# Kernel tuning notes

Hardware: AMD Instinct MI355X
Metric: run time of the kernel (lower is better)

Reference implementation:

```python
import jax, jax.numpy as jnp
import numpy as np

# Block sizes: 3-hop sampled bipartite graphs (src -> dst per layer)
N_SRC0, N_DST0, E0 = 500_000, 100_000, 1_000_000
N_DST1, E1 = 10_000, 100_000
N_DST2, E2 = 1_024, 10_240
D_IN, D_HID, N_CLS = 128, 128, 47


def setup_inputs() -> dict:
    key = jax.random.key(0)
    ks = jax.random.split(key, 16)
    feats = jax.random.normal(ks[0], (N_SRC0, D_IN), dtype=jnp.float32)
    src0 = jax.random.randint(ks[1], (E0,), 0, N_SRC0)
    dst0 = jax.random.randint(ks[2], (E0,), 0, N_DST0)
    src1 = jax.random.randint(ks[3], (E1,), 0, N_DST0)
    dst1 = jax.random.randint(ks[4], (E1,), 0, N_DST1)
    src2 = jax.random.randint(ks[5], (E2,), 0, N_DST1)
    dst2 = jax.random.randint(ks[6], (E2,), 0, N_DST2)
    # fsi.inverse_idx reindex + NPFeatureShuffle all-to-all -> two permutations
    inverse_idx = jax.random.permutation(ks[7], N_DST0)
    shuffle_idx = jax.random.permutation(ks[8], N_DST0)
    def glorot(k, fan_in, fan_out):
        lim = np.sqrt(6.0 / (fan_in + fan_out)).astype(np.float32)
        return jax.random.uniform(k, (fan_in, fan_out), jnp.float32, -lim, lim)
    W0 = glorot(ks[9], D_IN, D_HID)
    b0 = jnp.zeros((D_HID,), jnp.float32)
    W1 = glorot(ks[10], D_HID, D_HID)
    b1 = jnp.zeros((D_HID,), jnp.float32)
    W2 = glorot(ks[11], D_HID, N_CLS)
    b2 = jnp.zeros((N_CLS,), jnp.float32)
    return dict(feats=feats, src0=src0, dst0=dst0, src1=src1, dst1=dst1,
                src2=src2, dst2=dst2, inverse_idx=inverse_idx,
                shuffle_idx=shuffle_idx, W0=W0, b0=b0, W1=W1, b1=b1, W2=W2, b2=b2)


def _graph_conv(h_src, src, dst, n_src, n_dst, W, b, norm_both):
    # DGL GraphConv: optional D^{-1/2} on src, W, sum-aggregate over edges,
    # optional D^{-1/2} on dst, + bias. Degrees clamped to min 1.
    ones = jnp.ones(src.shape[0], dtype=h_src.dtype)
    if norm_both:
        out_deg = jax.ops.segment_sum(ones, src, num_segments=n_src)
        h_src = h_src * jax.lax.rsqrt(jnp.clip(out_deg, 1.0, None))[:, None]
    msgs = (h_src @ W)[src]                      # [E, d_out] gather
    agg = jax.ops.segment_sum(msgs, dst, num_segments=n_dst)  # scatter-add
    if norm_both:
        in_deg = jax.ops.segment_sum(ones, dst, num_segments=n_dst)
        agg = agg * jax.lax.rsqrt(jnp.clip(in_deg, 1.0, None))[:, None]
    return agg + b


def reference(feats, src0, dst0, src1, dst1, src2, dst2,
              inverse_idx, shuffle_idx, W0, b0, W1, b1, W2, b2):
    # layer 0: norm='none'
    h = _graph_conv(feats, src0, dst0, N_SRC0, N_DST0, W0, b0, norm_both=False)
    # fsi.inverse_idx reindex + NPFeatureShuffle (modeled as permutations)
    h = h[inverse_idx]
    h = h[shuffle_idx]
    h = jax.nn.relu(h)  # dropout is identity in eval
    # layer 1: norm='both'
    h = _graph_conv(h, src1, dst1, N_DST0, N_DST1, W1, b1, norm_both=True)
    h = jax.nn.relu(h)
    # layer 2: norm='both'
    h = _graph_conv(h, src2, dst2, N_DST1, N_DST2, W2, b2, norm_both=True)
    return h
```

## Files before the change

kernel.cpp:

```cpp
#include <hip/hip_runtime.h>
#include <stdint.h>

typedef unsigned int u32;
typedef unsigned short u16;
typedef __attribute__((ext_vector_type(8))) short short8;
typedef __attribute__((ext_vector_type(4))) float f32x4;

#define N_SRC0 500000
#define N_DST0 100000
#define N_DST1 10000
#define N_DST2 1024
#define NCLS 47
#define CAP 64

static __device__ __forceinline__ float bf16_lo(u32 v) { return __uint_as_float(v << 16); }
static __device__ __forceinline__ float bf16_hi(u32 v) { return __uint_as_float(v & 0xffff0000u); }
static __device__ __forceinline__ float bf16_to_f(u16 s) { return __uint_as_float(((u32)s) << 16); }
static __device__ __forceinline__ u16 f_to_bf16(float f) {
    u32 u = __float_as_uint(f);
    u32 r = u + 0x7fffu + ((u >> 16) & 1u);
    return (u16)(r >> 16);
}

#define OFF_X1     0u
#define OFF_X2     51200000u
#define OFF_CSR0   56320000u
#define OFF_CSR1   81920000u
#define OFF_CSR2   84480000u
#define OFF_CNT0   84742144u
#define OFF_DS1    85142144u
#define OFF_CNT1   85542144u
#define OFF_DS2    85582144u
#define OFF_CNT2   85622144u
#define ZERO_OFF   OFF_CNT0
#define ZERO_N4    55256u
#define OFF_WF0    85626240u
#define OFF_WF1    85691776u
#define OFF_WC2    85757312u
#define OFF_BC0    85781376u
#define OFF_BC1    85781888u
#define OFF_BC2    85782400u
#define OFF_FLAG   85782656u

__global__ __launch_bounds__(256) void k_prep(
    const u32* __restrict__ feats_w,
    const void* __restrict__ W0, const void* __restrict__ b0,
    const void* __restrict__ W1, const void* __restrict__ b1,
    const void* __restrict__ W2, const void* __restrict__ b2,
    float4* __restrict__ zbase,
    u16* __restrict__ wf0, u16* __restrict__ wf1,
    float* __restrict__ wc2, float* __restrict__ bc0,
    float* __restrict__ bc1, float* __restrict__ bc2,
    u32* __restrict__ flag)
{
    int b = blockIdx.x, t = threadIdx.x;
    if (b < 216) {
        u32 i = b * 256 + t;
        if (i < ZERO_N4) zbase[i] = make_float4(0.f, 0.f, 0.f, 0.f);
        return;
    }
    if (b == 216) {
        if (t < 64) {
            u32 u = feats_w[t];
            int e = (u >> 23) & 0xff;
            unsigned long long m = __ballot(e >= 0xC0);
            if (t == 0) *flag = (m != 0ull) ? 1u : 0u;
        }
        return;
    }
    __shared__ u32 lflag;
    if (b < 233) {
        const void* W = (b < 225) ? W0 : W1;
        u16* dst = (b < 225) ? wf0 : wf1;
        int base = ((b < 225) ? (b - 217) : (b - 225)) * 256;
        if (t == 0) lflag = 0u;
        __syncthreads();
        if (t < 64) { u32 u = ((const u32*)W)[t]; if (((u >> 23) & 0xff) >= 0xC0) atomicOr(&lflag, 1u); }
        __syncthreads();
        bool bf = (lflag != 0u);
        int idx = base + t;
        int fid = idx >> 6, lane = idx & 63;
        int nt = fid >> 2, ks = fid & 3;
        #pragma unroll
        for (int j = 0; j < 8; ++j) {
            int k = ks * 32 + (lane >> 4) * 8 + j;
            int n = nt * 16 + (lane & 15);
            u16 v = bf ? ((const u16*)W)[k * 128 + n]
                       : f_to_bf16(((const float*)W)[k * 128 + n]);
            dst[idx * 8 + j] = v;
        }
        return;
    }
    if (b < 257) {
        if (t == 0) lflag = 0u;
        __syncthreads();
        if (t < 64) { u32 u = ((const u32*)W2)[t]; if (((u >> 23) & 0xff) >= 0xC0) atomicOr(&lflag, 1u); }
        __syncthreads();
        bool bf = (lflag != 0u);
        int i = (b - 233) * 256 + t;
        if (i < 128 * NCLS)
            wc2[i] = bf ? bf16_to_f(((const u16*)W2)[i]) : ((const float*)W2)[i];
        return;
    }
    if (t < 128) { bc0[t] = ((const float*)b0)[t]; bc1[t] = ((const float*)b1)[t]; }
    if (t < NCLS) bc2[t] = ((const float*)b2)[t];
}

__global__ __launch_bounds__(256) void k_build(
    const int* __restrict__ src0, const int* __restrict__ dst0,
    const int* __restrict__ src1, const int* __restrict__ dst1,
    const int* __restrict__ src2, const int* __restrict__ dst2,
    u32* __restrict__ cnt0, int* __restrict__ csr0,
    u32* __restrict__ dS1,
    u32* __restrict__ cnt1, int* __restrict__ csr1,
    u32* __restrict__ dS2,
    u32* __restrict__ cnt2, int* __restrict__ csr2,
    int E0, int E1, int E2)
{
    int i = blockIdx.x * 256 + threadIdx.x;
    if (i < E0) {
        int d = dst0[i];
        u32 slot = atomicAdd(&cnt0[d], 1u);
        if (slot < CAP) csr0[d * CAP + slot] = src0[i];
    }
    if (i < E1) {
        atomicAdd(&dS1[src1[i]], 1u);
        int d = dst1[i];
        u32 slot = atomicAdd(&cnt1[d], 1u);
        if (slot < CAP) csr1[d * CAP + slot] = src1[i];
    }
    if (i < E2) {
        atomicAdd(&dS2[src2[i]], 1u);
        int d = dst2[i];
        u32 slot = atomicAdd(&cnt2[d], 1u);
        if (slot < CAP) csr2[d * CAP + slot] = src2[i];
    }
}

__global__ __launch_bounds__(256) void k_layer(
    const void* __restrict__ Ain, const u32* __restrict__ flag,
    const u32* __restrict__ cnt, const int* __restrict__ csr,
    const int* __restrict__ inv, const int* __restrict__ shuf,
    const u32* __restrict__ preDeg, const u32* __restrict__ postDeg,
    const u16* __restrict__ Wfrag, const float* __restrict__ bias,
    float* __restrict__ out, int rows)
{
    __shared__ u16  As[48][136];
    __shared__ u32  eS[48], degS[48];
    __shared__ float preS[48], postS[48], bS[128];

    int tid = threadIdx.x;
    int wv = tid >> 6, lane = tid & 63;
    int I0 = blockIdx.x * 48;

    if (tid < 48) {
        int I = I0 + tid;
        u32 e0 = 0u, dg = 0u; float pre = 1.f, post = 1.f;
        if (I < rows) {
            int ar = shuf ? inv[shuf[I]] : I;
            u32 c = cnt[ar];
            e0 = (u32)ar * CAP;
            dg = c < (u32)CAP ? c : (u32)CAP;
            if (preDeg)  { u32 d = preDeg[I];  pre  = rsqrtf((float)(d > 1u ? d : 1u)); }
            if (postDeg) { u32 d = postDeg[I]; post = rsqrtf((float)(d > 1u ? d : 1u)); }
        }
        eS[tid] = e0; degS[tid] = dg; preS[tid] = pre; postS[tid] = post;
    }
    if (tid < 128) bS[tid] = bias[tid];
    __syncthreads();

    bool bfp = flag && (*flag != 0u);

    for (int i = 0; i < 12; i += 3) {
        int rA = wv * 12 + i, rB = rA + 1, rC = rA + 2;
        int eA = (int)__builtin_amdgcn_readfirstlane(eS[rA]);
        int eB = (int)__builtin_amdgcn_readfirstlane(eS[rB]);
        int eC = (int)__builtin_amdgcn_readfirstlane(eS[rC]);
        int dA = (int)__builtin_amdgcn_readfirstlane(degS[rA]);
        int dB = (int)__builtin_amdgcn_readfirstlane(degS[rB]);
        int dC = (int)__builtin_amdgcn_readfirstlane(degS[rC]);
        int md = dA > dB ? dA : dB; md = md > dC ? md : dC;

        float xA = 0.f, yA = 0.f, xB = 0.f, yB = 0.f, xC = 0.f, yC = 0.f;

        if (bfp) {
            const u32* F = (const u32*)Ain;
            for (int k = 0; k < md; k += 8) {
                u32 vA[8], vB[8], vC[8];
                #pragma unroll
                for (int j = 0; j < 8; ++j) {
                    vA[j] = 0u;
                    if (k + j < dA) { int s = csr[eA + k + j]; vA[j] = F[(size_t)s * 64 + lane]; }
                }
                #pragma unroll
                for (int j = 0; j < 8; ++j) {
                    vB[j] = 0u;
                    if (k + j < dB) { int s = csr[eB + k + j]; vB[j] = F[(size_t)s * 64 + lane]; }
                }
                #pragma unroll
                for (int j = 0; j < 8; ++j) {
                    vC[j] = 0u;
                    if (k + j < dC) { int s = csr[eC + k + j]; vC[j] = F[(size_t)s * 64 + lane]; }
                }
                #pragma unroll
                for (int j = 0; j < 8; ++j) {
                    xA += bf16_lo(vA[j]); yA += bf16_hi(vA[j]);
                    xB += bf16_lo(vB[j]); yB += bf16_hi(vB[j]);
                    xC += bf16_lo(vC[j]); yC += bf16_hi(vC[j]);
                }
            }
        } else {
            const float2* F = (const float2*)Ain;
            for (int k = 0; k < md; k += 8) {
                float2 vA[8], vB[8], vC[8];
                #pragma unroll
                for (int j = 0; j < 8; ++j) {
                    vA[j] = make_float2(0.f, 0.f);
                    if (k + j < dA) { int s = csr[eA + k + j]; vA[j] = F[(size_t)s * 64 + lane]; }
                }
                #pragma unroll
                for (int j = 0; j < 8; ++j) {
                    vB[j] = make_float2(0.f, 0.f);
                    if (k + j < dB) { int s = csr[eB + k + j]; vB[j] = F[(size_t)s * 64 + lane]; }
                }
                #pragma unroll
                for (int j = 0; j < 8; ++j) {
                    vC[j] = make_float2(0.f, 0.f);
                    if (k + j < dC) { int s = csr[eC + k + j]; vC[j] = F[(size_t)s * 64 + lane]; }
                }
                #pragma unroll
                for (int j = 0; j < 8; ++j) {
                    xA += vA[j].x; yA += vA[j].y;
                    xB += vB[j].x; yB += vB[j].y;
                    xC += vC[j].x; yC += vC[j].y;
                }
            }
        }

        u32 pkA = ((u32)f_to_bf16(yA) << 16) | (u32)f_to_bf16(xA);
        u32 pkB = ((u32)f_to_bf16(yB) << 16) | (u32)f_to_bf16(xB);
        u32 pkC = ((u32)f_to_bf16(yC) << 16) | (u32)f_to_bf16(xC);
        *(u32*)&As[rA][2 * lane] = pkA;
        *(u32*)&As[rB][2 * lane] = pkB;
        *(u32*)&As[rC][2 * lane] = pkC;
    }

    short8 bfr[2][4];
    #pragma unroll
    for (int nt = 0; nt < 2; ++nt)
        #pragma unroll
        for (int ks = 0; ks < 4; ++ks) {
            int fid = (wv * 2 + nt) * 4 + ks;
            bfr[nt][ks] = *(const short8*)(Wfrag + (size_t)(fid * 64 + lane) * 8);
        }
    __syncthreads();

    f32x4 acc[2][3];
    #pragma unroll
    for (int nt = 0; nt < 2; ++nt)
        #pragma unroll
        for (int mt = 0; mt < 3; ++mt) acc[nt][mt] = (f32x4){0.f, 0.f, 0.f, 0.f};

    #pragma unroll
    for (int ks = 0; ks < 4; ++ks) {
        short8 af[3];
        #pragma unroll
        for (int mt = 0; mt < 3; ++mt) {
            int row = mt * 16 + (lane & 15);
            int k0 = ks * 32 + (lane >> 4) * 8;
            af[mt] = *(const short8*)&As[row][k0];
        }
        #pragma unroll
        for (int nt = 0; nt < 2; ++nt)
            #pragma unroll
            for (int mt = 0; mt < 3; ++mt)
                acc[nt][mt] = __builtin_amdgcn_mfma_f32_16x16x32_bf16(
                    af[mt], bfr[nt][ks], acc[nt][mt], 0, 0, 0);
    }

    int quad = lane >> 4, cl = lane & 15;
    #pragma unroll
    for (int nt = 0; nt < 2; ++nt) {
        int col = (wv * 2 + nt) * 16 + cl;
        float bb = bS[col];
        #pragma unroll
        for (int mt = 0; mt < 3; ++mt) {
            #pragma unroll
            for (int rg = 0; rg < 4; ++rg) {
                int lr = mt * 16 + quad * 4 + rg;
                int I = I0 + lr;
                if (I < rows) {
                    float v = acc[nt][mt][rg] * preS[lr] + bb;
                    v = v > 0.f ? v : 0.f;
                    out[(size_t)I * 128 + col] = v * postS[lr];
                }
            }
        }
    }
}

__global__ __launch_bounds__(256) void k_layer2(
    const float2* __restrict__ x2, const u32* __restrict__ cnt,
    const int* __restrict__ csr, const u32* __restrict__ preDeg,
    const float* __restrict__ Wc2, const float* __restrict__ bc2,
    void* __restrict__ out, const u32* __restrict__ flag)
{
    __shared__ float t2[16][128];
    int tid = threadIdx.x;
    int wv = tid >> 6, lane = tid & 63;
    int R0 = blockIdx.x * 16;

    for (int i = 0; i < 4; ++i) {
        int r = wv * 4 + i;
        int R = R0 + r;
        float x = 0.f, y = 0.f;
        u32 c = cnt[R];
        u32 e = (u32)R * CAP, end = e + (c < (u32)CAP ? c : (u32)CAP);
        for (; e + 4 <= end; e += 4) {
            int s0 = csr[e], s1 = csr[e+1], s2 = csr[e+2], s3 = csr[e+3];
            float2 v0 = x2[(size_t)s0 * 64 + lane];
            float2 v1 = x2[(size_t)s1 * 64 + lane];
            float2 v2 = x2[(size_t)s2 * 64 + lane];
            float2 v3 = x2[(size_t)s3 * 64 + lane];
            x += v0.x + v1.x + v2.x + v3.x;
            y += v0.y + v1.y + v2.y + v3.y;
        }
        for (; e < end; ++e) {
            float2 v = x2[(size_t)csr[e] * 64 + lane];
            x += v.x; y += v.y;
        }
        t2[r][2 * lane] = x;
        t2[r][2 * lane + 1] = y;
    }
    __syncthreads();

    bool bfp = flag && (*flag != 0u);
    for (int idx = tid; idx < 16 * NCLS; idx += 256) {
        int r = idx / NCLS, c = idx - NCLS * r;
        float a = 0.f;
        #pragma unroll 8
        for (int k = 0; k < 128; ++k) a = fmaf(t2[r][k], Wc2[k * NCLS + c], a);
        u32 d = preDeg[R0 + r];
        float v = a * rsqrtf((float)(d > 1u ? d : 1u)) + bc2[c];
        int g = (R0 + r) * NCLS + c;
        if (bfp) ((u16*)out)[g] = f_to_bf16(v);
        else     ((float*)out)[g] = v;
    }
}

extern "C" void kernel_launch(void* const* d_in, const int* in_sizes, int n_in,
                              void* d_out, int out_size, void* d_ws, size_t ws_size,
                              hipStream_t stream)
{
    (void)n_in; (void)out_size; (void)ws_size;
    const void* feats = d_in[0];
    const int* src0 = (const int*)d_in[1];
    const int* dst0 = (const int*)d_in[2];
    const int* src1 = (const int*)d_in[3];
    const int* dst1 = (const int*)d_in[4];
    const int* src2 = (const int*)d_in[5];
    const int* dst2 = (const int*)d_in[6];
    const int* inv  = (const int*)d_in[7];
    const int* shuf = (const int*)d_in[8];
    const void* W0 = d_in[9];  const void* b0 = d_in[10];
    const void* W1 = d_in[11]; const void* b1 = d_in[12];
    const void* W2 = d_in[13]; const void* b2 = d_in[14];
    int E0 = in_sizes[1], E1 = in_sizes[3], E2 = in_sizes[5];

    char* ws = (char*)d_ws;
    float* x1  = (float*)(ws + OFF_X1);
    float* x2  = (float*)(ws + OFF_X2);
    int* csr0 = (int*)(ws + OFF_CSR0);
    int* csr1 = (int*)(ws + OFF_CSR1);
    int* csr2 = (int*)(ws + OFF_CSR2);
    u32* cnt0 = (u32*)(ws + OFF_CNT0);
    u32* dS1  = (u32*)(ws + OFF_DS1);
    u32* cnt1 = (u32*)(ws + OFF_CNT1);
    u32* dS2  = (u32*)(ws + OFF_DS2);
    u32* cnt2 = (u32*)(ws + OFF_CNT2);
    u16* wf0  = (u16*)(ws + OFF_WF0);
    u16* wf1  = (u16*)(ws + OFF_WF1);
    float* wc2 = (float*)(ws + OFF_WC2);
    float* bc0 = (float*)(ws + OFF_BC0);
    float* bc1 = (float*)(ws + OFF_BC1);
    float* bc2 = (float*)(ws + OFF_BC2);
    u32* flag  = (u32*)(ws + OFF_FLAG);

    k_prep<<<258, 256, 0, stream>>>((const u32*)feats, W0, b0, W1, b1, W2, b2,
                                    (float4*)(ws + ZERO_OFF), wf0, wf1, wc2,
                                    bc0, bc1, bc2, flag);
    k_build<<<(E0 + 255) / 256, 256, 0, stream>>>(
        src0, dst0, src1, dst1, src2, dst2,
        cnt0, csr0, dS1, cnt1, csr1, dS2, cnt2, csr2, E0, E1, E2);
    k_layer<<<(N_DST0 + 47) / 48, 256, 0, stream>>>(
        feats, flag, cnt0, csr0, inv, shuf, nullptr, dS1, wf0, bc0, x1, N_DST0);
    k_layer<<<(N_DST1 + 47) / 48, 256, 0, stream>>>(
        x1, nullptr, cnt1, csr1, nullptr, nullptr, cnt1, dS2, wf1, bc1, x2, N_DST1);
    k_layer2<<<N_DST2 / 16, 256, 0, stream>>>(
        (const float2*)x2, cnt2, csr2, cnt2, wc2, bc2, d_out, flag);
}
```

Measured before the change: 554.3 us.

## Reorder layers to transform-then-aggregate with bf16 intermediate features

Splits each fused aggregate-then-GEMM layer into a dense GEMM kernel that projects every source row to bf16 first, followed by a gather/aggregate kernel that applies bias, ReLU and degree normalisation. The gathers for layers 0 and 1 now read bf16 projected rows instead of the raw inputs. The layer-1 activations are also stored as bf16 rather than fp32. In exchange the GEMM now runs over all 500k source rows instead of the 100k destinations, and the workspace grows by a large extra projected buffer, which adds streaming traffic.

```diff
diff --git a/kernel.cpp b/kernel.cpp
--- a/kernel.cpp
+++ b/kernel.cpp
@@ -22,25 +22,27 @@
     return (u16)(r >> 16);
 }
 
-#define OFF_X1     0u
-#define OFF_X2     51200000u
-#define OFF_CSR0   56320000u
-#define OFF_CSR1   81920000u
-#define OFF_CSR2   84480000u
-#define OFF_CNT0   84742144u
-#define OFF_DS1    85142144u
-#define OFF_CNT1   85542144u
-#define OFF_DS2    85582144u
-#define OFF_CNT2   85622144u
+#define OFF_Y0     0u
+#define OFF_X1     128004096u
+#define OFF_Y1     153604096u
+#define OFF_X2     179204096u
+#define OFF_CSR0   184324096u
+#define OFF_CSR1   209924096u
+#define OFF_CSR2   212484096u
+#define OFF_CNT0   212746240u
+#define OFF_DS1    213146240u
+#define OFF_CNT1   213546240u
+#define OFF_DS2    213586240u
+#define OFF_CNT2   213626240u
 #define ZERO_OFF   OFF_CNT0
 #define ZERO_N4    55256u
-#define OFF_WF0    85626240u
-#define OFF_WF1    85691776u
-#define OFF_WC2    85757312u
-#define OFF_BC0    85781376u
-#define OFF_BC1    85781888u
-#define OFF_BC2    85782400u
-#define OFF_FLAG   85782656u
+#define OFF_WF0    213630336u
+#define OFF_WF1    213695872u
+#define OFF_WC2    213761408u
+#define OFF_BC0    213785472u
+#define OFF_BC1    213785984u
+#define OFF_BC2    213786496u
+#define OFF_FLAG   213786752u
 
 __global__ __launch_bounds__(256) void k_prep(
     const u32* __restrict__ feats_w,
@@ -137,20 +139,104 @@
     }
 }
 
-__global__ __launch_bounds__(256) void k_layer(
-    const void* __restrict__ Ain, const u32* __restrict__ flag,
+__global__ __launch_bounds__(256) void k_gemm(
+    const void* __restrict__ Xin, const u32* __restrict__ flag, int isBf16In,
+    const u16* __restrict__ Wfrag, u16* __restrict__ Yout, int rows)
+{
+    __shared__ u16 As[48][136];
+    int tid = threadIdx.x, wv = tid >> 6, lane = tid & 63;
+    int I0 = blockIdx.x * 48;
+    bool bfp = flag ? (*flag != 0u) : (isBf16In != 0);
+
+    if (bfp) {
+        const uint4* F = (const uint4*)Xin;
+        for (int t = tid; t < 48 * 16; t += 256) {
+            int r = t >> 4, c = t & 15;
+            int I = I0 + r;
+            uint4 v = make_uint4(0u, 0u, 0u, 0u);
+            if (I < rows) v = F[(size_t)I * 16 + c];
+            *(uint4*)&As[r][c * 8] = v;
+        }
+    } else {
+        const float4* F = (const float4*)Xin;
+        for (int t = tid; t < 48 * 32; t += 256) {
+            int r = t >> 5, c = t & 31;
+            int I = I0 + r;
+            float4 v = make_float4(0.f, 0.f, 0.f, 0.f);
+            if (I < rows) v = F[(size_t)I * 32 + c];
+            u32 lo = ((u32)f_to_bf16(v.y) << 16) | (u32)f_to_bf16(v.x);
+            u32 hi = ((u32)f_to_bf16(v.w) << 16) | (u32)f_to_bf16(v.z);
+            *(u32*)&As[r][c * 4]     = lo;
+            *(u32*)&As[r][c * 4 + 2] = hi;
+        }
+    }
+
+    short8 bfr[2][4];
+    #pragma unroll
+    for (int nt = 0; nt < 2; ++nt)
+        #pragma unroll
+        for (int ks = 0; ks < 4; ++ks) {
+            int fid = (wv * 2 + nt) * 4 + ks;
+            bfr[nt][ks] = *(const short8*)(Wfrag + (size_t)(fid * 64 + lane) * 8);
+        }
+    __syncthreads();
+
+    f32x4 acc[2][3];
+    #pragma unroll
+    for (int nt = 0; nt < 2; ++nt)
+        #pragma unroll
+        for (int mt = 0; mt < 3; ++mt) acc[nt][mt] = (f32x4){0.f, 0.f, 0.f, 0.f};
+
+    #pragma unroll
+    for (int ks = 0; ks < 4; ++ks) {
+        short8 af[3];
+        #pragma unroll
+        for (int mt = 0; mt < 3; ++mt) {
+            int row = mt * 16 + (lane & 15);
+            int k0 = ks * 32 + (lane >> 4) * 8;
+            af[mt] = *(const short8*)&As[row][k0];
+        }
+        #pragma unroll
+        for (int nt = 0; nt < 2; ++nt)
+            #pragma unroll
+            for (int mt = 0; mt < 3; ++mt)
+                acc[nt][mt] = __builtin_amdgcn_mfma_f32_16x16x32_bf16(
+                    af[mt], bfr[nt][ks], acc[nt][mt], 0, 0, 0);
+    }
+    __syncthreads();
+
+    int quad = lane >> 4, cl = lane & 15;
+    #pragma unroll
+    for (int nt = 0; nt < 2; ++nt) {
+        int col = (wv * 2 + nt) * 16 + cl;
+        #pragma unroll
+        for (int mt = 0; mt < 3; ++mt)
+            #pragma unroll
+            for (int rg = 0; rg < 4; ++rg)
+                As[mt * 16 + quad * 4 + rg][col] = f_to_bf16(acc[nt][mt][rg]);
+    }
+    __syncthreads();
+
+    for (int t = tid; t < 48 * 16; t += 256) {
+        int r = t >> 4, c = t & 15;
+        int I = I0 + r;
+        if (I < rows)
+            *(uint4*)&Yout[(size_t)I * 128 + c * 8] = *(const uint4*)&As[r][c * 8];
+    }
+}
+
+__global__ __launch_bounds__(256) void k_agg(
+    const u32* __restrict__ Y,
     const u32* __restrict__ cnt, const int* __restrict__ csr,
     const int* __restrict__ inv, const int* __restrict__ shuf,
     const u32* __restrict__ preDeg, const u32* __restrict__ postDeg,
-    const u16* __restrict__ Wfrag, const float* __restrict__ bias,
-    float* __restrict__ out, int rows)
-{
-    __shared__ u16  As[48][136];
+    const float* __restrict__ bias, void* __restrict__ outp,
+    int outBf16, int rows)
+{
     __shared__ u32  eS[48], degS[48];
-    __shared__ float preS[48], postS[48], bS[128];
-
-    int tid = threadIdx.x;
-    int wv = tid >> 6, lane = tid & 63;
+    __shared__ float preS[48], postS[48];
+
+    int tid = threadIdx.x, wv = tid >> 6, lane = tid & 63;
     int I0 = blockIdx.x * 48;
 
     if (tid < 48) {
@@ -166,10 +252,9 @@
         }
         eS[tid] = e0; degS[tid] = dg; preS[tid] = pre; postS[tid] = post;
     }
-    if (tid < 128) bS[tid] = bias[tid];
     __syncthreads();
 
-    bool bfp = flag && (*flag != 0u);
+    float b0 = bias[2 * lane], b1 = bias[2 * lane + 1];
 
     for (int i = 0; i < 12; i += 3) {
         int rA = wv * 12 + i, rB = rA + 1, rC = rA + 2;
@@ -183,117 +268,46 @@
 
         float xA = 0.f, yA = 0.f, xB = 0.f, yB = 0.f, xC = 0.f, yC = 0.f;
 
-        if (bfp) {
-            const u32* F = (const u32*)Ain;
-            for (int k = 0; k < md; k += 8) {
-                u32 vA[8], vB[8], vC[8];
-                #pragma unroll
-                for (int j = 0; j < 8; ++j) {
-                    vA[j] = 0u;
-                    if (k + j < dA) { int s = csr[eA + k + j]; vA[j] = F[(size_t)s * 64 + lane]; }
-                }
-                #pragma unroll
-                for (int j = 0; j < 8; ++j) {
-                    vB[j] = 0u;
-                    if (k + j < dB) { int s = csr[eB + k + j]; vB[j] = F[(size_t)s * 64 + lane]; }
-                }
-                #pragma unroll
-                for (int j = 0; j < 8; ++j) {
-                    vC[j] = 0u;
-                    if (k + j < dC) { int s = csr[eC + k + j]; vC[j] = F[(size_t)s * 64 + lane]; }
-                }
-                #pragma unroll
-                for (int j = 0; j < 8; ++j) {
-                    xA += bf16_lo(vA[j]); yA += bf16_hi(vA[j]);
-                    xB += bf16_lo(vB[j]); yB += bf16_hi(vB[j]);
-                    xC += bf16_lo(vC[j]); yC += bf16_hi(vC[j]);
-                }
+        for (int k = 0; k < md; k += 8) {
+            u32 vA[8], vB[8], vC[8];
+            #pragma unroll
+            for (int j = 0; j < 8; ++j) {
+                vA[j] = 0u;
+                if (k + j < dA) { int s = csr[eA + k + j]; vA[j] = Y[(size_t)s * 64 + lane]; }
             }
-        } else {
-            const float2* F = (const float2*)Ain;
-            for (int k = 0; k < md; k += 8) {
-                float2 vA[8], vB[8], vC[8];
-                #pragma unroll
-                for (int j = 0; j < 8; ++j) {
-                    vA[j] = make_float2(0.f, 0.f);
-                    if (k + j < dA) { int s = csr[eA + k + j]; vA[j] = F[(size_t)s * 64 + lane]; }
-                }
-                #pragma unroll
-                for (int j = 0; j < 8; ++j) {
-                    vB[j] = make_float2(0.f, 0.f);
-                    if (k + j < dB) { int s = csr[eB + k + j]; vB[j] = F[(size_t)s * 64 + lane]; }
-                }
-                #pragma unroll
-                for (int j = 0; j < 8; ++j) {
-                    vC[j] = make_float2(0.f, 0.f);
-                    if (k + j < dC) { int s = csr[eC + k + j]; vC[j] = F[(size_t)s * 64 + lane]; }
-                }
-                #pragma unroll
-                for (int j = 0; j < 8; ++j) {
-                    xA += vA[j].x; yA += vA[j].y;
-                    xB += vB[j].x; yB += vB[j].y;
-                    xC += vC[j].x; yC += vC[j].y;
-                }
+            #pragma unroll
+            for (int j = 0; j < 8; ++j) {
+                vB[j] = 0u;
+                if (k + j < dB) { int s = csr[eB + k + j]; vB[j] = Y[(size_t)s * 64 + lane]; }
             }
-        }
-
-        u32 pkA = ((u32)f_to_bf16(yA) << 16) | (u32)f_to_bf16(xA);
-        u32 pkB = ((u32)f_to_bf16(yB) << 16) | (u32)f_to_bf16(xB);
-        u32 pkC = ((u32)f_to_bf16(yC) << 16) | (u32)f_to_bf16(xC);
-        *(u32*)&As[rA][2 * lane] = pkA;
-        *(u32*)&As[rB][2 * lane] = pkB;
-        *(u32*)&As[rC][2 * lane] = pkC;
-    }
-
-    short8 bfr[2][4];
-    #pragma unroll
-    for (int nt = 0; nt < 2; ++nt)
-        #pragma unroll
-        for (int ks = 0; ks < 4; ++ks) {
-            int fid = (wv * 2 + nt) * 4 + ks;
-            bfr[nt][ks] = *(const short8*)(Wfrag + (size_t)(fid * 64 + lane) * 8);
-        }
-    __syncthreads();
-
-    f32x4 acc[2][3];
-    #pragma unroll
-    for (int nt = 0; nt < 2; ++nt)
-        #pragma unroll
-        for (int mt = 0; mt < 3; ++mt) acc[nt][mt] = (f32x4){0.f, 0.f, 0.f, 0.f};
-
-    #pragma unroll
-    for (int ks = 0; ks < 4; ++ks) {
-        short8 af[3];
-        #pragma unroll
-        for (int mt = 0; mt < 3; ++mt) {
-            int row = mt * 16 + (lane & 15);
-            int k0 = ks * 32 + (lane >> 4) * 8;
-            af[mt] = *(const short8*)&As[row][k0];
-        }
-        #pragma unroll
-        for (int nt = 0; nt < 2; ++nt)
-            #pragma unroll
-            for (int mt = 0; mt < 3; ++mt)
-                acc[nt][mt] = __builtin_amdgcn_mfma_f32_16x16x32_bf16(
-                    af[mt], bfr[nt][ks], acc[nt][mt], 0, 0, 0);
-    }
-
-    int quad = lane >> 4, cl = lane & 15;
-    #pragma unroll
-    for (int nt = 0; nt < 2; ++nt) {
-        int col = (wv * 2 + nt) * 16 + cl;
-        float bb = bS[col];
-        #pragma unroll
-        for (int mt = 0; mt < 3; ++mt) {
-            #pragma unroll
-            for (int rg = 0; rg < 4; ++rg) {
-                int lr = mt * 16 + quad * 4 + rg;
-                int I = I0 + lr;
-                if (I < rows) {
-                    float v = acc[nt][mt][rg] * preS[lr] + bb;
-                    v = v > 0.f ? v : 0.f;
-                    out[(size_t)I * 128 + col] = v * postS[lr];
-                }
+            #pragma unroll
+            for (int j = 0; j < 8; ++j) {
+                vC[j] = 0u;
+                if (k + j < dC) { int s = csr[eC + k + j]; vC[j] = Y[(size_t)s * 64 + lane]; }
+            }
+            #pragma unroll
+            for (int j = 0; j < 8; ++j) {
+                xA += bf16_lo(vA[j]); yA += bf16_hi(vA[j]);
+                xB += bf16_lo(vB[j]); yB += bf16_hi(vB[j]);
+                xC += bf16_lo(vC[j]); yC += bf16_hi(vC[j]);
+            }
+        }
+
+        #pragma unroll
+        for (int p = 0; p < 3; ++p) {
+            int r = (p == 0) ? rA : (p == 1) ? rB : rC;
+            float sx = (p == 0) ? xA : (p == 1) ? xB : xC;
+            float sy = (p == 0) ? yA : (p == 1) ? yB : yC;
+            int I = I0 + r;
+            if (I < rows) {
+                float pre = preS[r], post = postS[r];
+                float vx = sx * pre + b0; vx = vx > 0.f ? vx : 0.f; vx *= post;
+                float vy = sy * pre + b1; vy = vy > 0.f ? vy : 0.f; vy *= post;
+                if (outBf16)
+                    ((u32*)outp)[(size_t)I * 64 + lane] =
+                        ((u32)f_to_bf16(vy) << 16) | (u32)f_to_bf16(vx);
+                else
+                    ((float2*)outp)[(size_t)I * 64 + lane] = make_float2(vx, vy);
             }
         }
     }
@@ -368,8 +382,10 @@
     int E0 = in_sizes[1], E1 = in_sizes[3], E2 = in_sizes[5];
 
     char* ws = (char*)d_ws;
-    float* x1  = (float*)(ws + OFF_X1);
-    float* x2  = (float*)(ws + OFF_X2);
+    u16* y0   = (u16*)(ws + OFF_Y0);
+    u16* x1   = (u16*)(ws + OFF_X1);
+    u16* y1   = (u16*)(ws + OFF_Y1);
+    float* x2 = (float*)(ws + OFF_X2);
     int* csr0 = (int*)(ws + OFF_CSR0);
     int* csr1 = (int*)(ws + OFF_CSR1);
     int* csr2 = (int*)(ws + OFF_CSR2);
@@ -392,10 +408,14 @@
     k_build<<<(E0 + 255) / 256, 256, 0, stream>>>(
         src0, dst0, src1, dst1, src2, dst2,
         cnt0, csr0, dS1, cnt1, csr1, dS2, cnt2, csr2, E0, E1, E2);
-    k_layer<<<(N_DST0 + 47) / 48, 256, 0, stream>>>(
-        feats, flag, cnt0, csr0, inv, shuf, nullptr, dS1, wf0, bc0, x1, N_DST0);
-    k_layer<<<(N_DST1 + 47) / 48, 256, 0, stream>>>(
-        x1, nullptr, cnt1, csr1, nullptr, nullptr, cnt1, dS2, wf1, bc1, x2, N_DST1);
+    k_gemm<<<(N_SRC0 + 47) / 48, 256, 0, stream>>>(
+        feats, flag, 0, wf0, y0, N_SRC0);
+    k_agg<<<(N_DST0 + 47) / 48, 256, 0, stream>>>(
+        (const u32*)y0, cnt0, csr0, inv, shuf, nullptr, dS1, bc0, x1, 1, N_DST0);
+    k_gemm<<<(N_DST0 + 47) / 48, 256, 0, stream>>>(
+        x1, nullptr, 1, wf1, y1, N_DST0);
+    k_agg<<<(N_DST1 + 47) / 48, 256, 0, stream>>>(
+        (const u32*)y1, cnt1, csr1, nullptr, nullptr, cnt1, dS2, bc1, x2, 0, N_DST1);
     k_layer2<<<N_DST2 / 16, 256, 0, stream>>>(
         (const float2*)x2, cnt2, csr2, cnt2, wc2, bc2, d_out, flag);
 }
```

Result: slower. 610.3 us (+10.1%).
